# Performance work log

Hardware: AMD Instinct MI355X
Metric: run time of the kernel (lower is better)

Reference implementation:

```python
import jax, jax.numpy as jnp
import numpy as np

N_NODES = 20000
N_EDGES = 640000
MUL = 32      # multiplicity of the 0e and 1o node-feature irreps
ATTR = 8      # node attr scalars (0e)
RBASIS = 16   # radial edge embedding size (0e)
FC_HID = 64   # radial MLP hidden size
AVG_NEIGH = 32.0
LOG2 = 0.6931471805599453


def _ssp(x):
    # ShiftedSoftPlus: softplus(x) - log(2)
    return jax.nn.softplus(x) - LOG2


def setup_inputs() -> dict:
    key = jax.random.key(0)
    ks = jax.random.split(key, 16)
    return {
        "node_s": jax.random.normal(ks[0], (N_NODES, MUL), jnp.float32),
        "node_v": jax.random.normal(ks[1], (N_NODES, MUL, 3), jnp.float32),
        "node_attrs": jax.random.uniform(ks[2], (N_NODES, ATTR), dtype=jnp.float32),
        "edge_emb": jax.random.normal(ks[3], (N_EDGES, RBASIS), jnp.float32),
        "edge_y0": jnp.ones((N_EDGES, 1), jnp.float32),  # Y_0 spherical harmonic is constant
        "edge_y1": jax.random.normal(ks[4], (N_EDGES, 3), jnp.float32),
        "edge_index": jax.random.randint(ks[5], (2, N_EDGES), 0, N_NODES, jnp.int32),
        "W1s": jax.random.normal(ks[6], (MUL, MUL), jnp.float32),
        "W1v": jax.random.normal(ks[7], (MUL, MUL), jnp.float32),
        "Wr1": jax.random.normal(ks[8], (RBASIS, FC_HID), jnp.float32),
        "Wr2": jax.random.normal(ks[9], (FC_HID, 4 * MUL), jnp.float32),
        "W2s": jax.random.normal(ks[10], (2 * MUL, MUL), jnp.float32),
        "W2v": jax.random.normal(ks[11], (2 * MUL, MUL), jnp.float32),
        "Wscs": jax.random.normal(ks[12], (MUL, ATTR, MUL), jnp.float32),
        "Wscv": jax.random.normal(ks[13], (MUL, ATTR, MUL), jnp.float32),
    }


def reference(node_s, node_v, node_attrs, edge_emb, edge_y0, edge_y1, edge_index,
              W1s, W1v, Wr1, Wr2, W2s, W2v, Wscs, Wscv):
    n = node_s.shape[0]
    src, dst = edge_index[0], edge_index[1]

    # linear_1 (e3nn Linear: per-irrep channel mixing, / sqrt(fan_in))
    inv_m = 1.0 / jnp.sqrt(jnp.float32(MUL))
    s = (node_s @ W1s) * inv_m                              # [N, MUL] 0e
    v = jnp.einsum('nui,uw->nwi', node_v, W1v) * inv_m      # [N, MUL, 3] 1o

    # radial MLP -> per-edge tensor-product weights (4 paths x MUL)
    h = _ssp((edge_emb @ Wr1) / jnp.sqrt(jnp.float32(RBASIS)))
    w = (h @ Wr2) / jnp.sqrt(jnp.float32(FC_HID))           # [E, 4*MUL]
    w1, w2, w3, w4 = jnp.split(w, 4, axis=1)

    # gather source node features
    se = s[src]                                             # [E, MUL]
    ve = v[src]                                             # [E, MUL, 3]

    # CG 'uvu' tensor product (sorted mid irreps: 0e(0ex0e), 0e(1ox1o), 1o(0ex1o), 1o(1ox0e))
    inv_sqrt3 = 1.0 / jnp.sqrt(3.0)
    mid_s = jnp.concatenate([
        w1 * se * edge_y0,                                          # 0e x 0e -> 0e
        w4 * jnp.einsum('eui,ei->eu', ve, edge_y1) * inv_sqrt3,     # 1o x 1o -> 0e
    ], axis=1)                                              # [E, 2*MUL]
    mid_v = jnp.concatenate([
        (w2 * se)[:, :, None] * edge_y1[:, None, :],                # 0e x 1o -> 1o
        w3[:, :, None] * ve * edge_y0[:, :, None],                  # 1o x 0e -> 1o
    ], axis=1)                                              # [E, 2*MUL, 3]

    # scatter-sum to destination nodes, / sqrt(avg_num_neighbors)
    inv_deg = 1.0 / jnp.sqrt(jnp.float32(AVG_NEIGH))
    agg_s = jax.ops.segment_sum(mid_s, dst, num_segments=n) * inv_deg
    agg_v = jax.ops.segment_sum(mid_v, dst, num_segments=n) * inv_deg

    # linear_2
    inv_2m = 1.0 / jnp.sqrt(jnp.float32(2 * MUL))
    ns = (agg_s @ W2s) * inv_2m
    nv = jnp.einsum('nui,uw->nwi', agg_v, W2v) * inv_2m

    # self connection: FullyConnectedTensorProduct(node_feats_in, node_attrs)
    inv_fan = 1.0 / jnp.sqrt(jnp.float32(MUL * ATTR))
    sc_s = jnp.einsum('nu,nv,uvw->nw', node_s, node_attrs, Wscs) * inv_fan
    sc_v = jnp.einsum('nui,nv,uvw->nwi', node_v, node_attrs, Wscv) * inv_fan

    out_s = ns + sc_s                                       # [N, MUL]
    out_v = (nv + sc_v).reshape(n, 3 * MUL)                 # [N, 3*MUL]
    return jnp.concatenate([out_s, out_v], axis=1)          # [N, 4*MUL] flat irreps layout
```

## Files before the change

kernel.cpp:

```cpp
#include <hip/hip_runtime.h>
#include <math.h>

typedef short bf16x8 __attribute__((ext_vector_type(8)));
typedef short short2v __attribute__((ext_vector_type(2)));
typedef short short4v __attribute__((ext_vector_type(4)));
typedef float f32x4 __attribute__((ext_vector_type(4)));

__device__ __forceinline__ float sspf(float x) {
    return __logf(1.0f + __expf(x)) - 0.6931471805599453f;
}
__device__ __forceinline__ short f2b(float f) {
    union { float f; unsigned u; } c; c.f = f;
    unsigned r = c.u + 0x7fff + ((c.u >> 16) & 1);
    return (short)(r >> 16);
}
__device__ __forceinline__ float b2f(short s) {
    union { unsigned u; float f; } c; c.u = ((unsigned)(unsigned short)s) << 16;
    return c.f;
}
__device__ __forceinline__ int rlanei(int v, int l) {
    return __builtin_amdgcn_readlane(v, l);
}
__device__ __forceinline__ float rlanef(float v, int l) {
    return __uint_as_float(__builtin_amdgcn_readlane(__float_as_uint(v), l));
}
__device__ __forceinline__ bf16x8 pack8(float4 a, float4 b) {
    bf16x8 o;
    o[0] = f2b(a.x); o[1] = f2b(a.y); o[2] = f2b(a.z); o[3] = f2b(a.w);
    o[4] = f2b(b.x); o[5] = f2b(b.y); o[6] = f2b(b.z); o[7] = f2b(b.w);
    return o;
}

constexpr float INV_M      = 0.17677669529663687f;
constexpr float INV_R      = 0.25f;
constexpr float INV_H      = 0.125f;
constexpr float INV_2M_DEG = 0.125f * 0.17677669529663687f;
constexpr float INV_FAN    = 0.0625f;
constexpr float INV_SQRT3  = 0.5773502691896258f;

__global__ __launch_bounds__(256) void k_lin1h(
    const float* __restrict__ node_s, const float* __restrict__ node_v,
    const float* __restrict__ W1s, const float* __restrict__ W1v,
    short* __restrict__ feat, int N,
    const int* __restrict__ eidx, int* __restrict__ count, int E,
    float4* __restrict__ aggz, int nagg4, int nblin, int nbhist)
{
    int b = blockIdx.x;
    int tid = threadIdx.x;
    if (b >= nblin + nbhist) {
        int i0 = (b - nblin - nbhist) * 1024 + tid;
        #pragma unroll
        for (int r = 0; r < 4; ++r) {
            int idx = i0 + r * 256;
            if (idx < nagg4) aggz[idx] = make_float4(0.f, 0.f, 0.f, 0.f);
        }
        return;
    }
    if (b >= nblin) {
        int e = (b - nblin) * 256 + tid;
        if (e < E) atomicAdd(&count[(eidx[E + e] << 2) | (e & 3)], 1);
        return;
    }
    __shared__ short sF[4 * 512];
    {
        int f = tid >> 6, ln = tid & 63;
        int q = ln >> 4, lm = ln & 15;
        int nt = f & 1;
        const float* Wp = (f < 2) ? W1s : W1v;
        short* d8 = &sF[tid * 8];
        #pragma unroll
        for (int j = 0; j < 8; ++j) {
            int k = q * 8 + j;
            d8[j] = f2b(Wp[k * 32 + nt * 16 + lm] * INV_M);
        }
    }
    __syncthreads();
    int lane = tid & 63, wv = tid >> 6;
    int q = lane >> 4, lm = lane & 15;
    int n0 = (b * 4 + wv) * 16;
    if (n0 >= N) return;
    int nr = n0 + lm;

    const float* nsp = node_s + (size_t)nr * 32;
    bf16x8 as8 = pack8(*(const float4*)(nsp + q * 8), *(const float4*)(nsp + q * 8 + 4));
    const float* nvp = node_v + (size_t)nr * 96;
    bf16x8 av8[3];
    #pragma unroll
    for (int i = 0; i < 3; ++i)
        #pragma unroll
        for (int j = 0; j < 8; ++j) av8[i][j] = f2b(nvp[(q * 8 + j) * 3 + i]);

    #pragma unroll
    for (int nt = 0; nt < 2; ++nt) {
        bf16x8 bs = *(const bf16x8*)&sF[(nt * 64 + lane) * 8];
        bf16x8 bv = *(const bf16x8*)&sF[((2 + nt) * 64 + lane) * 8];
        f32x4 sa = __builtin_amdgcn_mfma_f32_16x16x32_bf16(
            as8, bs, (f32x4){0.f, 0.f, 0.f, 0.f}, 0, 0, 0);
        f32x4 v0 = __builtin_amdgcn_mfma_f32_16x16x32_bf16(
            av8[0], bv, (f32x4){0.f, 0.f, 0.f, 0.f}, 0, 0, 0);
        f32x4 v1 = __builtin_amdgcn_mfma_f32_16x16x32_bf16(
            av8[1], bv, (f32x4){0.f, 0.f, 0.f, 0.f}, 0, 0, 0);
        f32x4 v2 = __builtin_amdgcn_mfma_f32_16x16x32_bf16(
            av8[2], bv, (f32x4){0.f, 0.f, 0.f, 0.f}, 0, 0, 0);
        #pragma unroll
        for (int r = 0; r < 4; ++r) {
            short4v o = {f2b(sa[r]), f2b(v0[r]), f2b(v1[r]), f2b(v2[r])};
            *(short4v*)&feat[(size_t)(n0 + q * 4 + r) * 128 + (nt * 16 + lm) * 4] = o;
        }
    }
}

__global__ __launch_bounds__(256) void k_scanA(
    const int* __restrict__ count, int* __restrict__ bsum, int M)
{
    int tid = threadIdx.x;
    int i = blockIdx.x * 256 + tid;
    int v = (i < M) ? count[i] : 0;
    int x = v;
    #pragma unroll
    for (int off = 1; off < 64; off <<= 1) x += __shfl_xor(x, off, 64);
    __shared__ int ws[4];
    int lane = tid & 63, wv = tid >> 6;
    if (lane == 0) ws[wv] = x;
    __syncthreads();
    if (tid == 0) bsum[blockIdx.x] = ws[0] + ws[1] + ws[2] + ws[3];
}

__global__ __launch_bounds__(512) void k_scanB(
    const int* __restrict__ bsum, int* __restrict__ boff, int NB)
{
    int tid = threadIdx.x;
    int v = (tid < NB) ? bsum[tid] : 0;
    int lane = tid & 63, wv = tid >> 6;
    int x = v;
    #pragma unroll
    for (int off = 1; off < 64; off <<= 1) {
        int y = __shfl_up(x, off, 64);
        if (lane >= off) x += y;
    }
    __shared__ int wsum[8], woff[8];
    if (lane == 63) wsum[wv] = x;
    __syncthreads();
    if (wv == 0 && lane < 8) {
        int t = wsum[lane];
        int xx = t;
        #pragma unroll
        for (int off = 1; off < 8; off <<= 1) {
            int y = __shfl_up(xx, off, 64);
            if (lane >= off) xx += y;
        }
        woff[lane] = xx - t;
    }
    __syncthreads();
    if (tid < NB) boff[tid] = x - v + woff[wv];
}

__global__ __launch_bounds__(256) void k_scanC(
    const int* __restrict__ count, const int* __restrict__ boff,
    int* __restrict__ cursor, int M)
{
    int tid = threadIdx.x;
    int i = blockIdx.x * 256 + tid;
    int v = (i < M) ? count[i] : 0;
    int lane = tid & 63, wv = tid >> 6;
    int x = v;
    #pragma unroll
    for (int off = 1; off < 64; off <<= 1) {
        int y = __shfl_up(x, off, 64);
        if (lane >= off) x += y;
    }
    __shared__ int wsum[4], woff2[4];
    if (lane == 63) wsum[wv] = x;
    __syncthreads();
    if (wv == 0 && lane < 4) {
        int t = wsum[lane];
        int xx = t;
        #pragma unroll
        for (int off = 1; off < 4; off <<= 1) {
            int y = __shfl_up(xx, off, 64);
            if (lane >= off) xx += y;
        }
        woff2[lane] = xx - t;
    }
    __syncthreads();
    if (i < M) cursor[i] = x - v + woff2[wv] + boff[blockIdx.x];
}

__global__ __launch_bounds__(256) void k_fill(
    const int* __restrict__ eidx, int* __restrict__ cursor,
    int2* __restrict__ epair, int E)
{
    int e = blockIdx.x * 256 + threadIdx.x;
    if (e < E) {
        int d = eidx[E + e];
        int slot = atomicAdd(&cursor[(d << 2) | (e & 3)], 1);
        epair[slot] = make_int2(e, d);
    }
}

__global__ __launch_bounds__(256) void k_fused(
    const float* __restrict__ emb, const int2* __restrict__ epair,
    const int* __restrict__ eidx, const float* __restrict__ y0v,
    const float* __restrict__ y1,
    const float* __restrict__ Wr1, const float* __restrict__ Wr2,
    const short* __restrict__ feat,
    float* __restrict__ agg_s, float* __restrict__ agg_v, int E)
{
    __shared__ short sW1[4 * 512];
    __shared__ short hbuf[4][16 * 72];
    __shared__ short wtl[4][2 * 64 * 18];

    int tid = threadIdx.x;
    {
        int f = tid >> 6, ln = tid & 63;
        int qq = ln >> 4, lmm = ln & 15;
        short* d8 = &sW1[(f * 64 + ln) * 8];
        #pragma unroll
        for (int j = 0; j < 8; ++j) {
            int k = qq * 8 + j;
            d8[j] = (k < 16) ? f2b(Wr1[k * 64 + f * 16 + lmm] * INV_R) : (short)0;
        }
    }
    __syncthreads();

    int lane = tid & 63, wv = tid >> 6;
    int q = lane >> 4, lm = lane & 15;
    int u = lane & 31;
    bool low = (lane < 32);

    bf16x8 wr2f[16];
    #pragma unroll
    for (int nt = 0; nt < 8; ++nt) {
        #pragma unroll
        for (int kc = 0; kc < 2; ++kc) {
            #pragma unroll
            for (int j = 0; j < 8; ++j) {
                int k = kc * 32 + q * 8 + j;
                wr2f[nt * 2 + kc][j] = f2b(Wr2[k * 128 + nt * 16 + lm] * INV_H);
            }
        }
    }

    short* hl = hbuf[wv];
    short* wl = wtl[wv];

    int base = blockIdx.x * 256 + wv * 64;
    if (base >= E) return;

    int2 nep = epair[base + lm];
    float4 pa = make_float4(0.f, 0.f, 0.f, 0.f);
    float4 pb = make_float4(0.f, 0.f, 0.f, 0.f);
    if (q < 2) {
        const float* ep = emb + (size_t)nep.x * 16 + q * 8;
        pa = *(const float4*)ep;
        pb = *(const float4*)(ep + 4);
    }
    int nsrc = 0;
    if (lane >= 16 && lane < 32) nsrc = eidx[nep.x];
    float npk = (q < 3) ? y1[(size_t)nep.x * 3 + q] : 0.f;

    float accs = 0.f, acc0 = 0.f, acc1 = 0.f, acc2 = 0.f;
    int cur = -1;

    for (int ch = 0; ch < 4; ++ch) {
        int2 myep = nep;
        int meta = (lane < 16) ? myep.y : nsrc;
        float pkm = npk;

        bf16x8 af = (bf16x8){0, 0, 0, 0, 0, 0, 0, 0};
        if (q < 2) af = pack8(pa, pb);

        short4v pg[8];
        #pragma unroll
        for (int k = 0; k < 8; ++k) {
            int sr = rlanei(meta, 16 + k);
            pg[k] = *(const short4v*)&feat[(size_t)sr * 128 + u * 4];
        }

        if (ch < 3) {
            nep = epair[base + ch * 16 + 16 + lm];
            if (q < 2) {
                const float* ep = emb + (size_t)nep.x * 16 + q * 8;
                pa = *(const float4*)ep;
                pb = *(const float4*)(ep + 4);
            }
            if (lane >= 16 && lane < 32) nsrc = eidx[nep.x];
            npk = (q < 3) ? y1[(size_t)nep.x * 3 + q] : 0.f;
        }

        #pragma unroll
        for (int nt = 0; nt < 4; ++nt) {
            bf16x8 bfr = *(const bf16x8*)&sW1[(nt * 64 + lane) * 8];
            f32x4 x = __builtin_amdgcn_mfma_f32_16x16x32_bf16(
                af, bfr, (f32x4){0.f, 0.f, 0.f, 0.f}, 0, 0, 0);
            #pragma unroll
            for (int r = 0; r < 4; ++r)
                hl[(q * 4 + r) * 72 + nt * 16 + lm] = f2b(sspf(x[r]));
        }

        bf16x8 ha = *(const bf16x8*)&hl[lm * 72 + q * 8];
        bf16x8 hb = *(const bf16x8*)&hl[lm * 72 + 32 + q * 8];
        #pragma unroll
        for (int nt = 0; nt < 8; ++nt) {
            f32x4 acc = __builtin_amdgcn_mfma_f32_16x16x32_bf16(
                ha, wr2f[nt * 2], (f32x4){0.f, 0.f, 0.f, 0.f}, 0, 0, 0);
            acc = __builtin_amdgcn_mfma_f32_16x16x32_bf16(hb, wr2f[nt * 2 + 1], acc, 0, 0, 0);
            float scl = (nt >= 6) ? INV_SQRT3 : 1.0f;
            int cp = (nt & 1) * 16 + lm + ((nt >> 2) & 1) * 32;
            int half = (nt >> 1) & 1;
            short* wp = &wl[half * 1152 + cp * 18 + q * 4];
            short2v p01 = {f2b(acc[0] * scl), f2b(acc[1] * scl)};
            short2v p23 = {f2b(acc[2] * scl), f2b(acc[3] * scl)};
            *(short2v*)&wp[0] = p01;
            *(short2v*)&wp[2] = p23;
        }

        #pragma unroll
        for (int i = 0; i < 16; ++i) {
            short4v g = pg[i & 7];
            if (i + 8 < 16) {
                int sr = rlanei(meta, 16 + i + 8);
                pg[(i + 8) & 7] = *(const short4v*)&feat[(size_t)sr * 128 + u * 4];
            }
            float se = b2f(g[0]), vx = b2f(g[1]), vy = b2f(g[2]), vz = b2f(g[3]);
            int d = rlanei(meta, i);
            if (d != cur) {
                if (cur >= 0) {
                    atomicAdd(&agg_s[(size_t)cur * 64 + lane], accs);
                    float* av = &agg_v[(size_t)cur * 192 + lane];
                    atomicAdd(av, acc0); atomicAdd(av + 64, acc1); atomicAdd(av + 128, acc2);
                }
                accs = acc0 = acc1 = acc2 = 0.f;
                cur = d;
            }
            float la = b2f(wl[lane * 18 + i]);
            float lb = b2f(wl[1152 + lane * 18 + i]);
            float y1x = rlanef(pkm, i);
            float y1y = rlanef(pkm, 16 + i);
            float y1z = rlanef(pkm, 32 + i);
            float dot = vx * y1x + vy * y1y + vz * y1z;
            accs = fmaf(low ? la : lb, low ? se : dot, accs);
            float t = low ? lb * se : la;
            acc0 = fmaf(t, low ? y1x : vx, acc0);
            acc1 = fmaf(t, low ? y1y : vy, acc1);
            acc2 = fmaf(t, low ? y1z : vz, acc2);
        }
    }
    if (cur >= 0) {
        atomicAdd(&agg_s[(size_t)cur * 64 + lane], accs);
        float* av = &agg_v[(size_t)cur * 192 + lane];
        atomicAdd(av, acc0); atomicAdd(av + 64, acc1); atomicAdd(av + 128, acc2);
    }
}

__global__ __launch_bounds__(256) void k_out(
    const float* __restrict__ node_s, const float* __restrict__ node_v,
    const float* __restrict__ attrs,
    const float* __restrict__ agg_s, const float* __restrict__ agg_v,
    const float* __restrict__ W2s, const float* __restrict__ W2v,
    const float* __restrict__ Wscs, const float* __restrict__ Wscv,
    float* __restrict__ out, int N)
{
    __shared__ short sB[40 * 512];
    int tid = threadIdx.x;
    for (int idx = tid; idx < 20480; idx += 256) {
        int f = idx >> 9, r = idx & 511;
        int j = r >> 6, ln = r & 63;
        int qq = ln >> 4, lmm = ln & 15;
        const float* Wp; int nt, t; float sc;
        if (f < 4)       { Wp = W2s;  nt = f >> 1;              t = f & 1; sc = INV_2M_DEG; }
        else if (f < 8)  { int g = f - 4;  Wp = W2v;  nt = g >> 1; t = g & 1; sc = INV_2M_DEG; }
        else if (f < 24) { int g = f - 8;  Wp = Wscs; nt = g >> 3; t = g & 7; sc = INV_FAN; }
        else             { int g = f - 24; Wp = Wscv; nt = g >> 3; t = g & 7; sc = INV_FAN; }
        sB[(f << 9) | (ln << 3) | j] =
            f2b(Wp[(t * 32 + qq * 8 + j) * 32 + nt * 16 + lmm] * sc);
    }
    __syncthreads();

    int lane = tid & 63, wv = tid >> 6;
    int q = lane >> 4, lm = lane & 15;
    int n0 = (blockIdx.x * 4 + wv) * 16;
    if (n0 >= N) return;
    int nr = n0 + lm;

    float4 at0 = *(const float4*)(attrs + (size_t)nr * 8);
    float4 at1 = *(const float4*)(attrs + (size_t)nr * 8 + 4);
    float at[8] = {at0.x, at0.y, at0.z, at0.w, at1.x, at1.y, at1.z, at1.w};

    const float* asp = agg_s + (size_t)nr * 64;
    bf16x8 aS[2];
    #pragma unroll
    for (int kc = 0; kc < 2; ++kc)
        aS[kc] = pack8(*(const float4*)(asp + kc * 32 + q * 8),
                       *(const float4*)(asp + kc * 32 + q * 8 + 4));

    const float* nsp = node_s + (size_t)nr * 32;
    bf16x8 scs[8];
    #pragma unroll
    for (int t = 0; t < 8; ++t) {
        float nv_ = nsp[t * 4 + q];
        #pragma unroll
        for (int j = 0; j < 8; ++j) scs[t][j] = f2b(nv_ * at[j]);
    }

    #pragma unroll
    for (int nt = 0; nt < 2; ++nt) {
        f32x4 acc = (f32x4){0.f, 0.f, 0.f, 0.f};
        acc = __builtin_amdgcn_mfma_f32_16x16x32_bf16(
            aS[0], *(const bf16x8*)&sB[(nt * 2 + 0) * 512 + lane * 8], acc, 0, 0, 0);
        acc = __builtin_amdgcn_mfma_f32_16x16x32_bf16(
            aS[1], *(const bf16x8*)&sB[(nt * 2 + 1) * 512 + lane * 8], acc, 0, 0, 0);
        #pragma unroll
        for (int t = 0; t < 8; ++t)
            acc = __builtin_amdgcn_mfma_f32_16x16x32_bf16(
                scs[t], *(const bf16x8*)&sB[(8 + nt * 8 + t) * 512 + lane * 8], acc, 0, 0, 0);
        #pragma unroll
        for (int r = 0; r < 4; ++r)
            out[(size_t)(n0 + q * 4 + r) * 128 + nt * 16 + lm] = acc[r];
    }

    const float* nvp = node_v + (size_t)nr * 96;
    const float* avp = agg_v + (size_t)nr * 192;
    #pragma unroll
    for (int i = 0; i < 3; ++i) {
        bf16x8 aV[2];
        #pragma unroll
        for (int kc = 0; kc < 2; ++kc)
            aV[kc] = pack8(*(const float4*)(avp + i * 64 + kc * 32 + q * 8),
                           *(const float4*)(avp + i * 64 + kc * 32 + q * 8 + 4));
        bf16x8 scv[8];
        #pragma unroll
        for (int t = 0; t < 8; ++t) {
            float nv_ = nvp[(t * 4 + q) * 3 + i];
            #pragma unroll
            for (int j = 0; j < 8; ++j) scv[t][j] = f2b(nv_ * at[j]);
        }
        #pragma unroll
        for (int nt = 0; nt < 2; ++nt) {
            f32x4 acc = (f32x4){0.f, 0.f, 0.f, 0.f};
            acc = __builtin_amdgcn_mfma_f32_16x16x32_bf16(
                aV[0], *(const bf16x8*)&sB[(4 + nt * 2 + 0) * 512 + lane * 8], acc, 0, 0, 0);
            acc = __builtin_amdgcn_mfma_f32_16x16x32_bf16(
                aV[1], *(const bf16x8*)&sB[(4 + nt * 2 + 1) * 512 + lane * 8], acc, 0, 0, 0);
            #pragma unroll
            for (int t = 0; t < 8; ++t)
                acc = __builtin_amdgcn_mfma_f32_16x16x32_bf16(
                    scv[t], *(const bf16x8*)&sB[(24 + nt * 8 + t) * 512 + lane * 8], acc, 0, 0, 0);
            #pragma unroll
            for (int r = 0; r < 4; ++r)
                out[(size_t)(n0 + q * 4 + r) * 128 + 32 + (nt * 16 + lm) * 3 + i] = acc[r];
        }
    }
}

extern "C" void kernel_launch(void* const* d_in, const int* in_sizes, int n_in,
                              void* d_out, int out_size, void* d_ws, size_t ws_size,
                              hipStream_t stream)
{
    const float* node_s = (const float*)d_in[0];
    const float* node_v = (const float*)d_in[1];
    const float* attrs  = (const float*)d_in[2];
    const float* emb    = (const float*)d_in[3];
    const float* y0     = (const float*)d_in[4];
    const float* y1     = (const float*)d_in[5];
    const int*   eidx   = (const int*)d_in[6];
    const float* W1s  = (const float*)d_in[7];
    const float* W1v  = (const float*)d_in[8];
    const float* Wr1  = (const float*)d_in[9];
    const float* Wr2  = (const float*)d_in[10];
    const float* W2s  = (const float*)d_in[11];
    const float* W2v  = (const float*)d_in[12];
    const float* Wscs = (const float*)d_in[13];
    const float* Wscv = (const float*)d_in[14];

    int N = in_sizes[0] / 32;
    int E = in_sizes[3] / 16;

    float* agg_s = (float*)d_ws;
    float* agg_v = agg_s + (size_t)N * 64;
    short* feat  = (short*)(agg_v + (size_t)N * 192);
    int* count   = (int*)(feat + (size_t)N * 128);
    int* cursor  = count + (size_t)4 * N;
    int2* epair  = (int2*)(cursor + (size_t)4 * N);
    int* bsum    = (int*)(epair + E);
    int* boff    = bsum + 1024;

    hipMemsetAsync(count, 0, (size_t)4 * N * sizeof(int), stream);

    int M  = 4 * N;
    int NB = (M + 255) / 256;
    int nblin  = (N + 63) / 64;
    int nbhist = (E + 255) / 256;
    int nagg4  = N * 64;
    int nbz    = (nagg4 + 1023) / 1024;
    k_lin1h<<<dim3(nblin + nbhist + nbz), dim3(256), 0, stream>>>(
        node_s, node_v, W1s, W1v, feat, N,
        eidx, count, E, (float4*)agg_s, nagg4, nblin, nbhist);
    k_scanA<<<dim3(NB), dim3(256), 0, stream>>>(count, bsum, M);
    k_scanB<<<dim3(1), dim3(512), 0, stream>>>(bsum, boff, NB);
    k_scanC<<<dim3(NB), dim3(256), 0, stream>>>(count, boff, cursor, M);
    k_fill<<<dim3((E + 255) / 256), dim3(256), 0, stream>>>(eidx, cursor, epair, E);
    k_fused<<<dim3((E + 255) / 256), dim3(256), 0, stream>>>(emb, epair, eidx, y0, y1,
                                                             Wr1, Wr2, feat,
                                                             agg_s, agg_v, E);
    k_out<<<dim3((N + 63) / 64), dim3(256), 0, stream>>>(node_s, node_v, attrs, agg_s, agg_v,
                                                         W2s, W2v, Wscs, Wscv, (float*)d_out, N);
}
```

Baseline: 327.8 us.

## Merge scan passes, pack src index into epair, pack edge weights in LDS

```diff
diff --git a/kernel.cpp b/kernel.cpp
--- a/kernel.cpp
+++ b/kernel.cpp
@@ -126,64 +126,37 @@
     if (tid == 0) bsum[blockIdx.x] = ws[0] + ws[1] + ws[2] + ws[3];
 }
 
-__global__ __launch_bounds__(512) void k_scanB(
-    const int* __restrict__ bsum, int* __restrict__ boff, int NB)
-{
-    int tid = threadIdx.x;
-    int v = (tid < NB) ? bsum[tid] : 0;
+__global__ __launch_bounds__(256) void k_scanC(
+    const int* __restrict__ count, const int* __restrict__ bsum,
+    int* __restrict__ cursor, int M)
+{
+    int tid = threadIdx.x, bid = blockIdx.x;
     int lane = tid & 63, wv = tid >> 6;
+    int p = 0;
+    if (tid < bid) p = bsum[tid];
+    if (tid + 256 < bid) p += bsum[tid + 256];
+    #pragma unroll
+    for (int off = 1; off < 64; off <<= 1) p += __shfl_xor(p, off, 64);
+    __shared__ int rs[4];
+    if (lane == 0) rs[wv] = p;
+    __syncthreads();
+    int boffv = rs[0] + rs[1] + rs[2] + rs[3];
+
+    int i = bid * 256 + tid;
+    int v = (i < M) ? count[i] : 0;
     int x = v;
     #pragma unroll
     for (int off = 1; off < 64; off <<= 1) {
         int y = __shfl_up(x, off, 64);
         if (lane >= off) x += y;
     }
-    __shared__ int wsum[8], woff[8];
+    __shared__ int wsum[4];
     if (lane == 63) wsum[wv] = x;
     __syncthreads();
-    if (wv == 0 && lane < 8) {
-        int t = wsum[lane];
-        int xx = t;
-        #pragma unroll
-        for (int off = 1; off < 8; off <<= 1) {
-            int y = __shfl_up(xx, off, 64);
-            if (lane >= off) xx += y;
-        }
-        woff[lane] = xx - t;
-    }
-    __syncthreads();
-    if (tid < NB) boff[tid] = x - v + woff[wv];
-}
-
-__global__ __launch_bounds__(256) void k_scanC(
-    const int* __restrict__ count, const int* __restrict__ boff,
-    int* __restrict__ cursor, int M)
-{
-    int tid = threadIdx.x;
-    int i = blockIdx.x * 256 + tid;
-    int v = (i < M) ? count[i] : 0;
-    int lane = tid & 63, wv = tid >> 6;
-    int x = v;
-    #pragma unroll
-    for (int off = 1; off < 64; off <<= 1) {
-        int y = __shfl_up(x, off, 64);
-        if (lane >= off) x += y;
-    }
-    __shared__ int wsum[4], woff2[4];
-    if (lane == 63) wsum[wv] = x;
-    __syncthreads();
-    if (wv == 0 && lane < 4) {
-        int t = wsum[lane];
-        int xx = t;
-        #pragma unroll
-        for (int off = 1; off < 4; off <<= 1) {
-            int y = __shfl_up(xx, off, 64);
-            if (lane >= off) xx += y;
-        }
-        woff2[lane] = xx - t;
-    }
-    __syncthreads();
-    if (i < M) cursor[i] = x - v + woff2[wv] + boff[blockIdx.x];
+    int add = 0;
+    #pragma unroll
+    for (int w = 0; w < 3; ++w) if (w < wv) add += wsum[w];
+    if (i < M) cursor[i] = x - v + add + boffv;
 }
 
 __global__ __launch_bounds__(256) void k_fill(
@@ -193,14 +166,14 @@
     int e = blockIdx.x * 256 + threadIdx.x;
     if (e < E) {
         int d = eidx[E + e];
+        int s = eidx[e];
         int slot = atomicAdd(&cursor[(d << 2) | (e & 3)], 1);
-        epair[slot] = make_int2(e, d);
+        epair[slot] = make_int2(e, d | (s << 16));
     }
 }
 
 __global__ __launch_bounds__(256) void k_fused(
     const float* __restrict__ emb, const int2* __restrict__ epair,
-    const int* __restrict__ eidx, const float* __restrict__ y0v,
     const float* __restrict__ y1,
     const float* __restrict__ Wr1, const float* __restrict__ Wr2,
     const short* __restrict__ feat,
@@ -208,7 +181,7 @@
 {
     __shared__ short sW1[4 * 512];
     __shared__ short hbuf[4][16 * 72];
-    __shared__ short wtl[4][2 * 64 * 18];
+    __shared__ int   wtl[4][64 * 17];
 
     int tid = threadIdx.x;
     {
@@ -231,18 +204,19 @@
     bf16x8 wr2f[16];
     #pragma unroll
     for (int nt = 0; nt < 8; ++nt) {
+        float sc = INV_H * ((nt >= 6) ? INV_SQRT3 : 1.0f);
         #pragma unroll
         for (int kc = 0; kc < 2; ++kc) {
             #pragma unroll
             for (int j = 0; j < 8; ++j) {
                 int k = kc * 32 + q * 8 + j;
-                wr2f[nt * 2 + kc][j] = f2b(Wr2[k * 128 + nt * 16 + lm] * INV_H);
+                wr2f[nt * 2 + kc][j] = f2b(Wr2[k * 128 + nt * 16 + lm] * sc);
             }
         }
     }
 
     short* hl = hbuf[wv];
-    short* wl = wtl[wv];
+    int* wli = wtl[wv];
 
     int base = blockIdx.x * 256 + wv * 64;
     if (base >= E) return;
@@ -255,8 +229,6 @@
         pa = *(const float4*)ep;
         pb = *(const float4*)(ep + 4);
     }
-    int nsrc = 0;
-    if (lane >= 16 && lane < 32) nsrc = eidx[nep.x];
     float npk = (q < 3) ? y1[(size_t)nep.x * 3 + q] : 0.f;
 
     float accs = 0.f, acc0 = 0.f, acc1 = 0.f, acc2 = 0.f;
@@ -264,7 +236,7 @@
 
     for (int ch = 0; ch < 4; ++ch) {
         int2 myep = nep;
-        int meta = (lane < 16) ? myep.y : nsrc;
+        int meta = (lane < 16) ? (myep.y & 0xffff) : (int)(((unsigned)myep.y) >> 16);
         float pkm = npk;
 
         bf16x8 af = (bf16x8){0, 0, 0, 0, 0, 0, 0, 0};
@@ -284,7 +256,6 @@
                 pa = *(const float4*)ep;
                 pb = *(const float4*)(ep + 4);
             }
-            if (lane >= 16 && lane < 32) nsrc = eidx[nep.x];
             npk = (q < 3) ? y1[(size_t)nep.x * 3 + q] : 0.f;
         }
 
@@ -301,18 +272,21 @@
         bf16x8 ha = *(const bf16x8*)&hl[lm * 72 + q * 8];
         bf16x8 hb = *(const bf16x8*)&hl[lm * 72 + 32 + q * 8];
         #pragma unroll
-        for (int nt = 0; nt < 8; ++nt) {
-            f32x4 acc = __builtin_amdgcn_mfma_f32_16x16x32_bf16(
-                ha, wr2f[nt * 2], (f32x4){0.f, 0.f, 0.f, 0.f}, 0, 0, 0);
-            acc = __builtin_amdgcn_mfma_f32_16x16x32_bf16(hb, wr2f[nt * 2 + 1], acc, 0, 0, 0);
-            float scl = (nt >= 6) ? INV_SQRT3 : 1.0f;
-            int cp = (nt & 1) * 16 + lm + ((nt >> 2) & 1) * 32;
-            int half = (nt >> 1) & 1;
-            short* wp = &wl[half * 1152 + cp * 18 + q * 4];
-            short2v p01 = {f2b(acc[0] * scl), f2b(acc[1] * scl)};
-            short2v p23 = {f2b(acc[2] * scl), f2b(acc[3] * scl)};
-            *(short2v*)&wp[0] = p01;
-            *(short2v*)&wp[2] = p23;
+        for (int pr = 0; pr < 4; ++pr) {
+            int ntA = (pr & 1) | ((pr >> 1) << 2);
+            int ntB = ntA + 2;
+            f32x4 aA = __builtin_amdgcn_mfma_f32_16x16x32_bf16(
+                ha, wr2f[ntA * 2], (f32x4){0.f, 0.f, 0.f, 0.f}, 0, 0, 0);
+            aA = __builtin_amdgcn_mfma_f32_16x16x32_bf16(hb, wr2f[ntA * 2 + 1], aA, 0, 0, 0);
+            f32x4 aB = __builtin_amdgcn_mfma_f32_16x16x32_bf16(
+                ha, wr2f[ntB * 2], (f32x4){0.f, 0.f, 0.f, 0.f}, 0, 0, 0);
+            aB = __builtin_amdgcn_mfma_f32_16x16x32_bf16(hb, wr2f[ntB * 2 + 1], aB, 0, 0, 0);
+            int cp = (pr & 1) * 16 + lm + (pr >> 1) * 32;
+            int* wp = &wli[cp * 17 + q * 4];
+            #pragma unroll
+            for (int r = 0; r < 4; ++r)
+                wp[r] = (int)(((unsigned)(unsigned short)f2b(aA[r])) |
+                              (((unsigned)(unsigned short)f2b(aB[r])) << 16));
         }
 
         #pragma unroll
@@ -333,8 +307,9 @@
                 accs = acc0 = acc1 = acc2 = 0.f;
                 cur = d;
             }
-            float la = b2f(wl[lane * 18 + i]);
-            float lb = b2f(wl[1152 + lane * 18 + i]);
+            unsigned wword = (unsigned)wli[lane * 17 + i];
+            float la = __uint_as_float(wword << 16);
+            float lb = __uint_as_float(wword & 0xffff0000u);
             float y1x = rlanef(pkm, i);
             float y1y = rlanef(pkm, 16 + i);
             float y1z = rlanef(pkm, 32 + i);
@@ -461,7 +436,6 @@
     const float* node_v = (const float*)d_in[1];
     const float* attrs  = (const float*)d_in[2];
     const float* emb    = (const float*)d_in[3];
-    const float* y0     = (const float*)d_in[4];
     const float* y1     = (const float*)d_in[5];
     const int*   eidx   = (const int*)d_in[6];
     const float* W1s  = (const float*)d_in[7];
@@ -483,7 +457,6 @@
     int* cursor  = count + (size_t)4 * N;
     int2* epair  = (int2*)(cursor + (size_t)4 * N);
     int* bsum    = (int*)(epair + E);
-    int* boff    = bsum + 1024;
 
     hipMemsetAsync(count, 0, (size_t)4 * N * sizeof(int), stream);
 
@@ -497,10 +470,9 @@
         node_s, node_v, W1s, W1v, feat, N,
         eidx, count, E, (float4*)agg_s, nagg4, nblin, nbhist);
     k_scanA<<<dim3(NB), dim3(256), 0, stream>>>(count, bsum, M);
-    k_scanB<<<dim3(1), dim3(512), 0, stream>>>(bsum, boff, NB);
-    k_scanC<<<dim3(NB), dim3(256), 0, stream>>>(count, boff, cursor, M);
+    k_scanC<<<dim3(NB), dim3(256), 0, stream>>>(count, bsum, cursor, M);
     k_fill<<<dim3((E + 255) / 256), dim3(256), 0, stream>>>(eidx, cursor, epair, E);
-    k_fused<<<dim3((E + 255) / 256), dim3(256), 0, stream>>>(emb, epair, eidx, y0, y1,
+    k_fused<<<dim3((E + 255) / 256), dim3(256), 0, stream>>>(emb, epair, y1,
                                                              Wr1, Wr2, feat,
                                                              agg_s, agg_v, E);
     k_out<<<dim3((N + 63) / 64), dim3(256), 0, stream>>>(node_s, node_v, attrs, agg_s, agg_v,
```

Result: slower. 335.7 us (+2.4%).
